# Kernel tuning notes

Hardware: AMD Instinct MI355X
Metric: run time of the kernel (lower is better)

## Reference

```python
import jax, jax.numpy as jnp
import numpy as np

B, N, D = 16, 1024, 768
SCALE = D ** (-0.5)


def setup_inputs() -> dict:
    key = jax.random.key(0)
    ks = jax.random.split(key, 6)
    return {
        "x": jax.random.normal(ks[0], (B, N, D), dtype=jnp.float32),
        "y": jax.random.normal(ks[1], (B, N, D), dtype=jnp.float32),
        "coords": jax.random.normal(ks[2], (N, N, 6), dtype=jnp.float32),
        "W_qk": jax.random.normal(ks[3], (D, D), dtype=jnp.float32) * (D ** -0.5),
        "pos_emb": jax.random.normal(ks[4], (N, 6, 1), dtype=jnp.float32) * 0.02,
        "gating": jnp.float32(1.0),
        "temp": jnp.float32(0.1),
    }


def reference(x, y, coords, W_qk, pos_emb, gating, temp):
    # k = Linear(y), no bias; torch Linear: y @ W.T
    k = jnp.einsum('bnd,ed->bne', y, W_qk)
    # content score [B, N, N]
    patch_score = jax.nn.softmax(jnp.einsum('bnd,bmd->bnm', x, k) * SCALE, axis=-1)
    # positional score: coords [N, N, 6] @ pos_emb [N, 6, 1] -> [N, N]
    pos_score = jax.nn.softmax(jnp.einsum('pnk,pkl->pnl', coords, pos_emb)[..., 0], axis=-1)
    g = jax.nn.sigmoid(gating)
    attn = (1.0 - g) * patch_score + g * pos_score[None, :, :]  # broadcast over B
    out = jnp.einsum('bnm,bmd->bnd', attn, y)
    entropy = jnp.sum(-attn * jnp.log(attn + 1e-8), axis=-1, keepdims=True)  # [B, N, 1]
    hmap = 2.0 * (1.0 - jax.nn.sigmoid(temp * entropy))
    return out, hmap
```

## Files before the change

kernel.cpp:

```cpp
#include <hip/hip_runtime.h>
#include <hip/hip_bf16.h>
#include <cstdint>

typedef __bf16 bf16_t;
typedef __bf16 bf16x8 __attribute__((ext_vector_type(8)));
typedef __bf16 bf16x4 __attribute__((ext_vector_type(4)));
typedef float f32x4 __attribute__((ext_vector_type(4)));

static constexpr int B = 16, N = 1024, D = 768;
static constexpr float SCALE = 0.03608439182435161f;

#define ASYNC_COPY16(gptr, lptr)                                                          \
  __builtin_amdgcn_global_load_lds((const __attribute__((address_space(1))) void*)(gptr), \
                                   (__attribute__((address_space(3))) void*)(lptr), 16, 0, 0)

__device__ __forceinline__ float wave_red_max(float v) {
#pragma unroll
  for (int o = 32; o > 0; o >>= 1) v = fmaxf(v, __shfl_down(v, o, 64));
  return v;
}
__device__ __forceinline__ float wave_red_sum(float v) {
#pragma unroll
  for (int o = 32; o > 0; o >>= 1) v += __shfl_down(v, o, 64);
  return v;
}
__device__ __forceinline__ float block_max(float v, float* sm) {
  v = wave_red_max(v);
  int lane = threadIdx.x & 63, w = threadIdx.x >> 6;
  if (lane == 0) sm[w] = v;
  __syncthreads();
  return fmaxf(fmaxf(sm[0], sm[1]), fmaxf(sm[2], sm[3]));
}
__device__ __forceinline__ float block_sum(float v, float* sm) {
  v = wave_red_sum(v);
  int lane = threadIdx.x & 63, w = threadIdx.x >> 6;
  if (lane == 0) sm[w] = v;
  __syncthreads();
  return sm[0] + sm[1] + sm[2] + sm[3];
}

__global__ __launch_bounds__(256) void cast_f32_bf16_4(const float4* __restrict__ in,
                                                       bf16x4* __restrict__ out, int n4) {
  int i = blockIdx.x * 256 + threadIdx.x;
  if (i < n4) {
    float4 v = in[i];
    bf16x4 o;
    o.x = (bf16_t)v.x; o.y = (bf16_t)v.y; o.z = (bf16_t)v.z; o.w = (bf16_t)v.w;
    out[i] = o;
  }
}

__global__ __launch_bounds__(256) void cast_transpose_y(const float* __restrict__ y,
                                                        bf16_t* __restrict__ yb,
                                                        bf16_t* __restrict__ yT) {
  __shared__ bf16_t t[32][33];
  int b = blockIdx.z;
  int d0 = blockIdx.x * 32;
  int n0 = blockIdx.y * 32;
  int tx = threadIdx.x & 31;
  int ty = threadIdx.x >> 5;
  const float* src = y + (size_t)b * N * D;
  bf16_t* dstN = yb + (size_t)b * N * D;
  bf16_t* dstT = yT + (size_t)b * N * D;
#pragma unroll
  for (int r = 0; r < 4; r++) {
    int n = n0 + ty + r * 8;
    float v = src[(size_t)n * D + d0 + tx];
    bf16_t h = (bf16_t)v;
    t[ty + r * 8][tx] = h;
    dstN[(size_t)n * D + d0 + tx] = h;
  }
  __syncthreads();
#pragma unroll
  for (int r = 0; r < 4; r++) {
    int d = d0 + ty + r * 8;
    dstT[(size_t)d * N + n0 + tx] = t[tx][ty + r * 8];
  }
}

__global__ __launch_bounds__(256) void pos_softmax_k(const float* __restrict__ coords,
                                                     const float* __restrict__ pemb,
                                                     float* __restrict__ pos) {
  __shared__ float sm1[4], sm2[4];
  int p = blockIdx.x;
  int tid = threadIdx.x;
  float e[6];
#pragma unroll
  for (int k = 0; k < 6; k++) e[k] = pemb[p * 6 + k];
  float v[4];
#pragma unroll
  for (int i = 0; i < 4; i++) {
    int n = tid + i * 256;
    const float* c = coords + ((size_t)p * N + n) * 6;
    float s = 0.f;
#pragma unroll
    for (int k = 0; k < 6; k++) s += c[k] * e[k];
    v[i] = s;
  }
  float m = block_max(fmaxf(fmaxf(v[0], v[1]), fmaxf(v[2], v[3])), sm1);
  float ex[4], ls = 0.f;
#pragma unroll
  for (int i = 0; i < 4; i++) { ex[i] = __expf(v[i] - m); ls += ex[i]; }
  float sum = block_sum(ls, sm2);
  float inv = 1.f / sum;
#pragma unroll
  for (int i = 0; i < 4; i++) pos[(size_t)p * N + tid + i * 256] = ex[i] * inv;
}

__global__ __launch_bounds__(256) void attn_entropy_k(float* __restrict__ S,
                                                      const float* __restrict__ pos,
                                                      const float* __restrict__ gating,
                                                      const float* __restrict__ temp,
                                                      float* __restrict__ hmap) {
  __shared__ float sm1[4], sm2[4], sm3[4];
  size_t row = blockIdx.x;
  int q = (int)(row & (size_t)(N - 1));
  int tid = threadIdx.x;
  float* Srow = S + row * N;
  float g = 1.f / (1.f + __expf(-gating[0]));
  float s[4];
#pragma unroll
  for (int i = 0; i < 4; i++) s[i] = Srow[tid + i * 256];
  float m = block_max(fmaxf(fmaxf(s[0], s[1]), fmaxf(s[2], s[3])), sm1);
  float e[4], ls = 0.f;
#pragma unroll
  for (int i = 0; i < 4; i++) { e[i] = __expf(s[i] - m); ls += e[i]; }
  float sum = block_sum(ls, sm2);
  float inv = 1.f / sum;
  const float* prow = pos + (size_t)q * N;
  float a[4], ent = 0.f;
#pragma unroll
  for (int i = 0; i < 4; i++) {
    float patch = e[i] * inv;
    float ps = prow[tid + i * 256];
    a[i] = (1.f - g) * patch + g * ps;
    ent += -a[i] * __logf(a[i] + 1e-8f);
  }
  float E = block_sum(ent, sm3);
  __syncthreads();
  bf16_t* arow = (bf16_t*)Srow;
#pragma unroll
  for (int i = 0; i < 4; i++) arow[tid + i * 256] = (bf16_t)a[i];
  if (tid == 0) hmap[row] = 2.f / (1.f + __expf(temp[0] * E));
}

template <typename OutT>
__global__ __launch_bounds__(512) void gemm_nt_256(const bf16_t* __restrict__ A, int lda, long long sA,
                                                   const bf16_t* __restrict__ Bm, int ldb, long long sB,
                                                   OutT* __restrict__ C, int ldc, long long sC,
                                                   int K, float scale, int swz) {
  __shared__ __align__(16) char lds_raw[98304];

  const int tid = threadIdx.x;
  const int lane = tid & 63, wave = tid >> 6;
  const int wr = wave >> 1, wc = wave & 1;
  const int quad = lane >> 4, lr = lane & 15;

  int bx = blockIdx.x, by = blockIdx.y, bz = blockIdx.z;
  if (swz) {
    int Gx = gridDim.x, Gy = gridDim.y, Gz = gridDim.z;
    int i = bx + Gx * (by + Gy * bz);
    int xcd = i & 7, slot = i >> 3;
    int T = Gx * Gy;
    int bpx = Gz >> 3;
    bz = xcd * bpx + slot / T;
    int t = slot % T;
    bx = t % Gx;
    by = t / Gx;
  }
  const int tileN = bx * 128, tileM = by * 256;
  A += (long long)bz * sA + (long long)tileM * lda;
  Bm += (long long)bz * sB + (long long)tileN * ldb;
  C += (long long)bz * sC;

  const bf16_t* ag = A + (long long)(wave * 32 + (lane >> 3)) * lda + (lane & 7) * 8;
  const bf16_t* bg = Bm + (long long)(wave * 16 + (lane >> 3)) * ldb + (lane & 7) * 8;

  f32x4 acc[4][4];
#pragma unroll
  for (int i = 0; i < 4; i++)
#pragma unroll
    for (int j = 0; j < 4; j++) acc[i][j] = (f32x4){0.f, 0.f, 0.f, 0.f};

  const int nk = K >> 6;

#pragma unroll
  for (int i = 0; i < 4; i++)
    ASYNC_COPY16(ag + (long long)i * 8 * lda, lds_raw + (wave * 32 + i * 8) * 128);
#pragma unroll
  for (int i = 0; i < 2; i++)
    ASYNC_COPY16(bg + (long long)i * 8 * ldb, lds_raw + 32768 + (wave * 16 + i * 8) * 128);
  __syncthreads();

  int cur = 0;
  for (int t = 0; t < nk; ++t) {
    if (t + 1 < nk) {
      char* nb = lds_raw + ((cur ^ 1) * 49152);
      const int kt = (t + 1) << 6;
#pragma unroll
      for (int i = 0; i < 4; i++)
        ASYNC_COPY16(ag + (long long)i * 8 * lda + kt, nb + (wave * 32 + i * 8) * 128);
#pragma unroll
      for (int i = 0; i < 2; i++)
        ASYNC_COPY16(bg + (long long)i * 8 * ldb + kt, nb + 32768 + (wave * 16 + i * 8) * 128);
    }
    const bf16_t* As = (const bf16_t*)(lds_raw + cur * 49152);
    const bf16_t* Bs = (const bf16_t*)(lds_raw + cur * 49152 + 32768);
#pragma unroll
    for (int kk = 0; kk < 2; kk++) {
      bf16x8 af[4], bfr[4];
#pragma unroll
      for (int i = 0; i < 4; i++) {
        af[i] = *(const bf16x8*)&As[(wr * 64 + i * 16 + lr) * 64 + kk * 32 + quad * 8];
        bfr[i] = *(const bf16x8*)&Bs[(wc * 64 + i * 16 + lr) * 64 + kk * 32 + quad * 8];
      }
#pragma unroll
      for (int mi = 0; mi < 4; mi++)
#pragma unroll
        for (int nj = 0; nj < 4; nj++)
          acc[mi][nj] = __builtin_amdgcn_mfma_f32_16x16x32_bf16(af[mi], bfr[nj], acc[mi][nj], 0, 0, 0);
    }
    __syncthreads();
    cur ^= 1;
  }

  float* epi = (float*)lds_raw + wave * (16 * 68);
#pragma unroll
  for (int mi = 0; mi < 4; mi++) {
#pragma unroll
    for (int nj = 0; nj < 4; nj++)
#pragma unroll
      for (int r = 0; r < 4; r++)
        epi[(quad * 4 + r) * 68 + nj * 16 + lr] = acc[mi][nj][r] * scale;
    if constexpr (sizeof(OutT) == 4) {
#pragma unroll
      for (int seg = 0; seg < 4; seg++) {
        int lrow = seg * 4 + (lane >> 4);
        f32x4 v = *(const f32x4*)&epi[lrow * 68 + (lane & 15) * 4];
        long long grow = tileM + wr * 64 + mi * 16 + lrow;
        int gcol = tileN + wc * 64 + (lane & 15) * 4;
        *(f32x4*)&C[grow * ldc + gcol] = v;
      }
    } else {
#pragma unroll
      for (int seg = 0; seg < 2; seg++) {
        int lrow = seg * 8 + (lane >> 3);
        const float* p = &epi[lrow * 68 + (lane & 7) * 8];
        f32x4 v0 = *(const f32x4*)&p[0];
        f32x4 v1 = *(const f32x4*)&p[4];
        bf16x8 o;
#pragma unroll
        for (int j = 0; j < 4; j++) { o[j] = (bf16_t)v0[j]; o[j + 4] = (bf16_t)v1[j]; }
        long long grow = tileM + wr * 64 + mi * 16 + lrow;
        int gcol = tileN + wc * 64 + (lane & 7) * 8;
        *(bf16x8*)&C[grow * ldc + gcol] = o;
      }
    }
  }
}

extern "C" void kernel_launch(void* const* d_in, const int* in_sizes, int n_in,
                              void* d_out, int out_size, void* d_ws, size_t ws_size,
                              hipStream_t stream) {
  const float* x = (const float*)d_in[0];
  const float* y = (const float*)d_in[1];
  const float* coords = (const float*)d_in[2];
  const float* W = (const float*)d_in[3];
  const float* pemb = (const float*)d_in[4];
  const float* gating = (const float*)d_in[5];
  const float* temp = (const float*)d_in[6];
  float* out = (float*)d_out;
  float* hmap = out + (size_t)B * N * D;

  char* ws = (char*)d_ws;
  bf16_t* xb = (bf16_t*)(ws + 0);
  bf16_t* yb = (bf16_t*)(ws + 25165824);
  bf16_t* yT = (bf16_t*)(ws + 50331648);
  bf16_t* Wb = (bf16_t*)(ws + 75497472);
  bf16_t* kb = (bf16_t*)(ws + 76677120);
  float* pos = (float*)(ws + 101842944);
  float* S   = (float*)(ws + 106037248);

  const int BND = B * N * D;

  cast_f32_bf16_4<<<BND / 4 / 256, 256, 0, stream>>>((const float4*)x, (bf16x4*)xb, BND / 4);
  cast_f32_bf16_4<<<(D * D / 4 + 255) / 256, 256, 0, stream>>>((const float4*)W, (bf16x4*)Wb, D * D / 4);
  cast_transpose_y<<<dim3(D / 32, N / 32, B), 256, 0, stream>>>(y, yb, yT);
  pos_softmax_k<<<N, 256, 0, stream>>>(coords, pemb, pos);

  gemm_nt_256<bf16_t><<<dim3(D / 128, (B * N) / 256, 1), 512, 0, stream>>>(
      yb, D, 0LL, Wb, D, 0LL, kb, D, 0LL, D, 1.0f, 0);

  gemm_nt_256<float><<<dim3(N / 128, N / 256, B), 512, 0, stream>>>(
      xb, D, (long long)N * D, kb, D, (long long)N * D, S, N, (long long)N * N, D, SCALE, 1);

  attn_entropy_k<<<B * N, 256, 0, stream>>>(S, pos, gating, temp, hmap);

  gemm_nt_256<float><<<dim3(D / 128, N / 256, B), 512, 0, stream>>>(
      (const bf16_t*)S, 2 * N, (long long)N * 2 * N, yT, N, (long long)N * D, out, D, (long long)N * D, N, 1.0f, 1);
}
```

Before: 341.1 us.

## Rewrite GEMM as 256x256 tile with 8-phase interleaved prefetch schedule

```diff
diff --git a/kernel.cpp b/kernel.cpp
--- a/kernel.cpp
+++ b/kernel.cpp
@@ -145,15 +145,15 @@
 }
 
 template <typename OutT>
-__global__ __launch_bounds__(512) void gemm_nt_256(const bf16_t* __restrict__ A, int lda, long long sA,
-                                                   const bf16_t* __restrict__ Bm, int ldb, long long sB,
-                                                   OutT* __restrict__ C, int ldc, long long sC,
-                                                   int K, float scale, int swz) {
-  __shared__ __align__(16) char lds_raw[98304];
+__global__ __launch_bounds__(512, 1) void gemm_nt_8p(const bf16_t* __restrict__ A, int lda, long long sA,
+                                                     const bf16_t* __restrict__ Bm, int ldb, long long sB,
+                                                     OutT* __restrict__ C, int ldc, long long sC,
+                                                     int K, float scale, int swz) {
+  __shared__ __align__(16) char lds_raw[131072];
 
   const int tid = threadIdx.x;
   const int lane = tid & 63, wave = tid >> 6;
-  const int wr = wave >> 1, wc = wave & 1;
+  const int wr = wave >> 2, wc = wave & 3;
   const int quad = lane >> 4, lr = lane & 15;
 
   int bx = blockIdx.x, by = blockIdx.y, bz = blockIdx.z;
@@ -168,76 +168,118 @@
     bx = t % Gx;
     by = t / Gx;
   }
-  const int tileN = bx * 128, tileM = by * 256;
+  const int tileN = bx * 256, tileM = by * 256;
   A += (long long)bz * sA + (long long)tileM * lda;
   Bm += (long long)bz * sB + (long long)tileN * ldb;
   C += (long long)bz * sC;
 
-  const bf16_t* ag = A + (long long)(wave * 32 + (lane >> 3)) * lda + (lane & 7) * 8;
-  const bf16_t* bg = Bm + (long long)(wave * 16 + (lane >> 3)) * ldb + (lane & 7) * 8;
-
-  f32x4 acc[4][4];
-#pragma unroll
-  for (int i = 0; i < 4; i++)
+  const bf16_t* a_src = A + (long long)(tid >> 3) * lda + (tid & 7) * 8;
+  const bf16_t* b_src = Bm + (long long)(tid >> 3) * ldb + (tid & 7) * 8;
+
+  auto STAGE_A = [&](int t, int h) {
+    char* base = lds_raw + (t & 1) * 65536 + h * 16384 + wave * 1024;
+    const bf16_t* g = a_src + (long long)(h * 128) * lda + t * 64;
+    ASYNC_COPY16(g, base);
+    ASYNC_COPY16(g + (long long)64 * lda, base + 8192);
+  };
+  auto STAGE_B = [&](int t, int h) {
+    char* base = lds_raw + (t & 1) * 65536 + 32768 + h * 16384 + wave * 1024;
+    const bf16_t* g = b_src + (long long)(h * 128) * ldb + t * 64;
+    ASYNC_COPY16(g, base);
+    ASYNC_COPY16(g + (long long)64 * ldb, base + 8192);
+  };
+
+  f32x4 acc[8][4];
+#pragma unroll
+  for (int i = 0; i < 8; i++)
 #pragma unroll
     for (int j = 0; j < 4; j++) acc[i][j] = (f32x4){0.f, 0.f, 0.f, 0.f};
 
   const int nk = K >> 6;
-
-#pragma unroll
-  for (int i = 0; i < 4; i++)
-    ASYNC_COPY16(ag + (long long)i * 8 * lda, lds_raw + (wave * 32 + i * 8) * 128);
-#pragma unroll
-  for (int i = 0; i < 2; i++)
-    ASYNC_COPY16(bg + (long long)i * 8 * ldb, lds_raw + 32768 + (wave * 16 + i * 8) * 128);
-  __syncthreads();
-
-  int cur = 0;
-  for (int t = 0; t < nk; ++t) {
-    if (t + 1 < nk) {
-      char* nb = lds_raw + ((cur ^ 1) * 49152);
-      const int kt = (t + 1) << 6;
-#pragma unroll
-      for (int i = 0; i < 4; i++)
-        ASYNC_COPY16(ag + (long long)i * 8 * lda + kt, nb + (wave * 32 + i * 8) * 128);
-#pragma unroll
-      for (int i = 0; i < 2; i++)
-        ASYNC_COPY16(bg + (long long)i * 8 * ldb + kt, nb + 32768 + (wave * 16 + i * 8) * 128);
+  const int niter = nk >> 1;
+
+  STAGE_A(0, 0); STAGE_A(0, 1); STAGE_B(0, 0); STAGE_B(0, 1);
+  STAGE_B(1, 0); STAGE_B(1, 1);
+  asm volatile("s_waitcnt vmcnt(4)" ::: "memory");
+  __builtin_amdgcn_s_barrier();
+
+  for (int it = 0; it < niter; ++it) {
+    const int t1 = 2 * it + 1;
+    const bool pf = (t1 + 1) < nk;
+    bf16x8 bfr[4][2];
+#pragma unroll
+    for (int q = 0; q < 8; ++q) {
+      const int hb = q >> 2, qq = q & 3;
+      const bf16_t* As = (const bf16_t*)(lds_raw + hb * 65536 + wr * 16384);
+      const bf16_t* Bs = (const bf16_t*)(lds_raw + hb * 65536 + 32768 + (wc >> 1) * 16384);
+      if (qq == 0) {
+#pragma unroll
+        for (int nj = 0; nj < 4; ++nj)
+#pragma unroll
+          for (int kk = 0; kk < 2; ++kk)
+            bfr[nj][kk] = *(const bf16x8*)&Bs[((wc & 1) * 64 + nj * 16 + lr) * 64 + kk * 32 + quad * 8];
+      }
+      bf16x8 af[2][2];
+#pragma unroll
+      for (int s = 0; s < 2; ++s)
+#pragma unroll
+        for (int kk = 0; kk < 2; ++kk)
+          af[s][kk] = *(const bf16x8*)&As[((qq * 2 + s) * 16 + lr) * 64 + kk * 32 + quad * 8];
+      if (q == 0) {
+        STAGE_A(t1, 0);
+      } else if (q == 1) {
+        STAGE_A(t1, 1);
+      } else if (q == 2) {
+        if (pf) STAGE_B(t1 + 1, 0);
+      } else if (q == 3) {
+        if (pf) {
+          STAGE_B(t1 + 1, 1);
+          asm volatile("s_waitcnt vmcnt(4)" ::: "memory");
+        } else {
+          asm volatile("s_waitcnt vmcnt(0)" ::: "memory");
+        }
+      } else if (q == 4) {
+        if (pf) STAGE_A(t1 + 1, 0);
+      } else if (q == 5) {
+        if (pf) STAGE_A(t1 + 1, 1);
+      } else if (q == 6) {
+        if (pf) STAGE_B(t1 + 2, 0);
+      } else {
+        if (pf) {
+          STAGE_B(t1 + 2, 1);
+          asm volatile("s_waitcnt vmcnt(4)" ::: "memory");
+        }
+      }
+      __builtin_amdgcn_s_barrier();
+      __builtin_amdgcn_s_setprio(1);
+#pragma unroll
+      for (int s = 0; s < 2; ++s)
+#pragma unroll
+        for (int nj = 0; nj < 4; ++nj)
+#pragma unroll
+          for (int kk = 0; kk < 2; ++kk)
+            acc[qq * 2 + s][nj] =
+                __builtin_amdgcn_mfma_f32_16x16x32_bf16(af[s][kk], bfr[nj][kk], acc[qq * 2 + s][nj], 0, 0, 0);
+      __builtin_amdgcn_s_setprio(0);
+      __builtin_amdgcn_s_barrier();
     }
-    const bf16_t* As = (const bf16_t*)(lds_raw + cur * 49152);
-    const bf16_t* Bs = (const bf16_t*)(lds_raw + cur * 49152 + 32768);
-#pragma unroll
-    for (int kk = 0; kk < 2; kk++) {
-      bf16x8 af[4], bfr[4];
-#pragma unroll
-      for (int i = 0; i < 4; i++) {
-        af[i] = *(const bf16x8*)&As[(wr * 64 + i * 16 + lr) * 64 + kk * 32 + quad * 8];
-        bfr[i] = *(const bf16x8*)&Bs[(wc * 64 + i * 16 + lr) * 64 + kk * 32 + quad * 8];
-      }
-#pragma unroll
-      for (int mi = 0; mi < 4; mi++)
-#pragma unroll
-        for (int nj = 0; nj < 4; nj++)
-          acc[mi][nj] = __builtin_amdgcn_mfma_f32_16x16x32_bf16(af[mi], bfr[nj], acc[mi][nj], 0, 0, 0);
-    }
-    __syncthreads();
-    cur ^= 1;
-  }
+  }
+  __syncthreads();
 
   float* epi = (float*)lds_raw + wave * (16 * 68);
 #pragma unroll
-  for (int mi = 0; mi < 4; mi++) {
-#pragma unroll
-    for (int nj = 0; nj < 4; nj++)
-#pragma unroll
-      for (int r = 0; r < 4; r++)
+  for (int mi = 0; mi < 8; ++mi) {
+#pragma unroll
+    for (int nj = 0; nj < 4; ++nj)
+#pragma unroll
+      for (int r = 0; r < 4; ++r)
         epi[(quad * 4 + r) * 68 + nj * 16 + lr] = acc[mi][nj][r] * scale;
     if constexpr (sizeof(OutT) == 4) {
 #pragma unroll
       for (int seg = 0; seg < 4; seg++) {
         int lrow = seg * 4 + (lane >> 4);
         f32x4 v = *(const f32x4*)&epi[lrow * 68 + (lane & 15) * 4];
-        long long grow = tileM + wr * 64 + mi * 16 + lrow;
+        long long grow = tileM + wr * 128 + mi * 16 + lrow;
         int gcol = tileN + wc * 64 + (lane & 15) * 4;
         *(f32x4*)&C[grow * ldc + gcol] = v;
       }
@@ -251,7 +293,7 @@
         bf16x8 o;
 #pragma unroll
         for (int j = 0; j < 4; j++) { o[j] = (bf16_t)v0[j]; o[j + 4] = (bf16_t)v1[j]; }
-        long long grow = tileM + wr * 64 + mi * 16 + lrow;
+        long long grow = tileM + wr * 128 + mi * 16 + lrow;
         int gcol = tileN + wc * 64 + (lane & 7) * 8;
         *(bf16x8*)&C[grow * ldc + gcol] = o;
       }
@@ -288,14 +330,14 @@
   cast_transpose_y<<<dim3(D / 32, N / 32, B), 256, 0, stream>>>(y, yb, yT);
   pos_softmax_k<<<N, 256, 0, stream>>>(coords, pemb, pos);
 
-  gemm_nt_256<bf16_t><<<dim3(D / 128, (B * N) / 256, 1), 512, 0, stream>>>(
+  gemm_nt_8p<bf16_t><<<dim3(D / 256, (B * N) / 256, 1), 512, 0, stream>>>(
       yb, D, 0LL, Wb, D, 0LL, kb, D, 0LL, D, 1.0f, 0);
 
-  gemm_nt_256<float><<<dim3(N / 128, N / 256, B), 512, 0, stream>>>(
+  gemm_nt_8p<float><<<dim3(N / 256, N / 256, B), 512, 0, stream>>>(
       xb, D, (long long)N * D, kb, D, (long long)N * D, S, N, (long long)N * N, D, SCALE, 1);
 
   attn_entropy_k<<<B * N, 256, 0, stream>>>(S, pos, gating, temp, hmap);
 
-  gemm_nt_256<float><<<dim3(D / 128, N / 256, B), 512, 0, stream>>>(
+  gemm_nt_8p<float><<<dim3(D / 256, N / 256, B), 512, 0, stream>>>(
       (const bf16_t*)S, 2 * N, (long long)N * 2 * N, yT, N, (long long)N * D, out, D, (long long)N * D, N, 1.0f, 1);
 }
```

Result: faster. 316.8 us (-7.1%).
